# Optimization experiments

Measured on AMD Instinct MI355X. Metric: run time of the kernel, lower is better.

Reference implementation:

```python
import jax, jax.numpy as jnp
import numpy as np

E = 64          # num_experts
DIM = 1024      # model dim
HID = 512       # per-expert FFN hidden dim
N = 65536       # total routed tokens (1024 per expert)


def setup_inputs() -> dict:
    key = jax.random.key(0)
    k_x, k1, k2, k3 = jax.random.split(key, 4)
    x = jax.random.normal(k_x, (N, DIM), dtype=jnp.float32)
    # learned params: w1/w3 [E, HID, DIM], w2 [E, DIM, HID] (trunc_normal std 0.02 ~ normal*0.02)
    w1 = jax.random.normal(k1, (E, HID, DIM), dtype=jnp.float32) * 0.02
    w2 = jax.random.normal(k2, (E, DIM, HID), dtype=jnp.float32) * 0.02
    w3 = jax.random.normal(k3, (E, HID, DIM), dtype=jnp.float32) * 0.02
    num_tokens_per_expert = jnp.full((E,), N // E, dtype=jnp.int32)
    return {"x": x, "w1": w1, "w2": w2, "w3": w3,
            "num_tokens_per_expert": num_tokens_per_expert}


def reference(x, w1, w2, w3, num_tokens_per_expert):
    # Grouped-GEMM SwiGLU expert FFN (torch._grouped_mm path, bf16 compute).
    bf16 = jnp.bfloat16
    xb = x.astype(bf16)                                   # [N, DIM]
    g = num_tokens_per_expert                             # [E] int32 group sizes
    w1t = jnp.swapaxes(w1.astype(bf16), 1, 2)             # [E, DIM, HID]
    w3t = jnp.swapaxes(w3.astype(bf16), 1, 2)             # [E, DIM, HID]
    w2t = jnp.swapaxes(w2.astype(bf16), 1, 2)             # [E, HID, DIM]
    h = jax.nn.silu(jax.lax.ragged_dot(xb, w1t, g))       # [N, HID]
    h = h * jax.lax.ragged_dot(xb, w3t, g)                # fused gate
    out = jax.lax.ragged_dot(h, w2t, g)                   # [N, DIM]
    return out.astype(x.dtype)
```

## Files before the change

kernel.cpp:

```cpp
#include <hip/hip_runtime.h>
#include <hip/hip_bf16.h>
#include <stdint.h>

#define NE   64
#define DIM  1024
#define HID  512
#define TPE  1024

typedef __attribute__((ext_vector_type(8)))  __bf16          bf16x8;
typedef __attribute__((ext_vector_type(16))) float           f32x16;
typedef __attribute__((ext_vector_type(8)))  unsigned short  ushort8_t;
typedef __attribute__((ext_vector_type(4)))  float           float4_t;

__device__ __forceinline__ unsigned short f2bf(float f) {
  return __builtin_bit_cast(unsigned short, static_cast<__bf16>(f));
}
__device__ __forceinline__ float bf2f(unsigned short u) {
  unsigned int x = ((unsigned int)u) << 16;
  return __builtin_bit_cast(float, x);
}
__device__ __forceinline__ ushort8_t pack8(float4_t a, float4_t b) {
  ushort8_t r;
  r[0] = f2bf(a[0]); r[1] = f2bf(a[1]); r[2] = f2bf(a[2]); r[3] = f2bf(a[3]);
  r[4] = f2bf(b[0]); r[5] = f2bf(b[1]); r[6] = f2bf(b[2]); r[7] = f2bf(b[3]);
  return r;
}

#define LDK 40

__device__ __forceinline__ int xcd_swizzle(int bid, int nwg) {
  return (bid & 7) * (nwg >> 3) + (bid >> 3);
}

#define P1_NKT (DIM / 32)

__global__ __launch_bounds__(256, 4) void p1_kernel(
    const float* __restrict__ X, const float* __restrict__ W1,
    const float* __restrict__ W3, unsigned short* __restrict__ H) {
  __shared__ __align__(16) unsigned short lA [2][128 * LDK];
  __shared__ __align__(16) unsigned short lB1[2][ 64 * LDK];
  __shared__ __align__(16) unsigned short lB3[2][ 64 * LDK];

  const int tile = xcd_swizzle(blockIdx.x, NE * 8 * 8);
  const int e  = tile >> 6;
  const int tm = (tile >> 3) & 7;
  const int tn = tile & 7;
  const int t  = threadIdx.x;

  const float* gA  = X  + (size_t)(e * TPE + tm * 128) * DIM;
  const float* gB1 = W1 + ((size_t)e * HID + tn * 64) * DIM;
  const float* gB3 = W3 + ((size_t)e * HID + tn * 64) * DIM;

  float4_t ra[2][2], rb1[2], rb3[2];

  const int arow0 = t >> 2, acol = (t & 3) * 8;
  const int brow  = t >> 2, bcol = (t & 3) * 8;

  auto load_tile = [&](int kt) {
#pragma unroll
    for (int i = 0; i < 2; ++i) {
      const size_t off = (size_t)(arow0 + 64 * i) * DIM + kt * 32 + acol;
      ra[i][0] = *reinterpret_cast<const float4_t*>(gA + off);
      ra[i][1] = *reinterpret_cast<const float4_t*>(gA + off + 4);
    }
    const size_t boff = (size_t)brow * DIM + kt * 32 + bcol;
    rb1[0] = *reinterpret_cast<const float4_t*>(gB1 + boff);
    rb1[1] = *reinterpret_cast<const float4_t*>(gB1 + boff + 4);
    rb3[0] = *reinterpret_cast<const float4_t*>(gB3 + boff);
    rb3[1] = *reinterpret_cast<const float4_t*>(gB3 + boff + 4);
  };
  auto store_tile = [&](int buf) {
#pragma unroll
    for (int i = 0; i < 2; ++i)
      *reinterpret_cast<ushort8_t*>(&lA[buf][(arow0 + 64 * i) * LDK + acol]) =
          pack8(ra[i][0], ra[i][1]);
    *reinterpret_cast<ushort8_t*>(&lB1[buf][brow * LDK + bcol]) = pack8(rb1[0], rb1[1]);
    *reinterpret_cast<ushort8_t*>(&lB3[buf][brow * LDK + bcol]) = pack8(rb3[0], rb3[1]);
  };

  const int lane = t & 63;
  const int wv   = t >> 6;
  const int wr   = wv >> 1, wc = wv & 1;
  const int lr   = lane & 31;
  const int ks   = lane >> 5;

  const int aoff0 = (wr * 64 + lr) * LDK + ks * 8;
  const int boff0 = (wc * 32 + lr) * LDK + ks * 8;

  f32x16 acc1[2], acc3[2];
#pragma unroll
  for (int m = 0; m < 2; ++m)
#pragma unroll
    for (int i = 0; i < 16; ++i) { acc1[m][i] = 0.f; acc3[m][i] = 0.f; }

  load_tile(0);
  for (int kt = 0; kt < P1_NKT; ++kt) {
    const int buf = kt & 1;
    store_tile(buf);
    __syncthreads();
    if (kt + 1 < P1_NKT) load_tile(kt + 1);
#pragma unroll
    for (int kk = 0; kk < 2; ++kk) {
      bf16x8 a[2], b1, b3;
#pragma unroll
      for (int m = 0; m < 2; ++m)
        a[m] = __builtin_bit_cast(bf16x8, *reinterpret_cast<const ushort8_t*>(
                   &lA[buf][aoff0 + m * (32 * LDK) + kk * 16]));
      b1 = __builtin_bit_cast(bf16x8, *reinterpret_cast<const ushort8_t*>(
               &lB1[buf][boff0 + kk * 16]));
      b3 = __builtin_bit_cast(bf16x8, *reinterpret_cast<const ushort8_t*>(
               &lB3[buf][boff0 + kk * 16]));
#pragma unroll
      for (int m = 0; m < 2; ++m) {
        acc1[m] = __builtin_amdgcn_mfma_f32_32x32x16_bf16(a[m], b1, acc1[m], 0, 0, 0);
        acc3[m] = __builtin_amdgcn_mfma_f32_32x32x16_bf16(a[m], b3, acc3[m], 0, 0, 0);
      }
    }
  }

  const int tokBase = e * TPE + tm * 128 + wr * 64;
  const int hid     = tn * 64 + wc * 32 + lr;
#pragma unroll
  for (int m = 0; m < 2; ++m)
#pragma unroll
    for (int r = 0; r < 16; ++r) {
      const int rr  = (r & 3) + 8 * (r >> 2) + 4 * ks;
      const int tok = tokBase + m * 32 + rr;
      const float av = bf2f(f2bf(acc1[m][r]));
      const float bv = bf2f(f2bf(acc3[m][r]));
      const float s  = av / (1.0f + __expf(-av));
      H[(size_t)tok * HID + hid] = f2bf(s * bv);
    }
}

#define P2_NKT (HID / 32)

__global__ __launch_bounds__(256, 4) void p2_kernel(
    const unsigned short* __restrict__ Hin, const float* __restrict__ W2,
    float* __restrict__ OUT) {
  __shared__ __align__(16) unsigned short lA[2][128 * LDK];
  __shared__ __align__(16) unsigned short lB[2][128 * LDK];

  const int tile = xcd_swizzle(blockIdx.x, NE * 8 * 8);
  const int e  = tile >> 6;
  const int tm = (tile >> 3) & 7;
  const int tn = tile & 7;
  const int t  = threadIdx.x;

  const unsigned short* gA = Hin + (size_t)(e * TPE + tm * 128) * HID;
  const float*          gB = W2  + ((size_t)e * DIM + tn * 128) * HID;

  ushort8_t ra[2];
  float4_t  rb[2][2];

  const int row0 = t >> 2, col = (t & 3) * 8;

  auto load_tile = [&](int kt) {
#pragma unroll
    for (int i = 0; i < 2; ++i) {
      ra[i] = *reinterpret_cast<const ushort8_t*>(
          gA + (size_t)(row0 + 64 * i) * HID + kt * 32 + col);
      const size_t off = (size_t)(row0 + 64 * i) * HID + kt * 32 + col;
      rb[i][0] = *reinterpret_cast<const float4_t*>(gB + off);
      rb[i][1] = *reinterpret_cast<const float4_t*>(gB + off + 4);
    }
  };
  auto store_tile = [&](int buf) {
#pragma unroll
    for (int i = 0; i < 2; ++i) {
      const int idx = (row0 + 64 * i) * LDK + col;
      *reinterpret_cast<ushort8_t*>(&lA[buf][idx]) = ra[i];
      *reinterpret_cast<ushort8_t*>(&lB[buf][idx]) = pack8(rb[i][0], rb[i][1]);
    }
  };

  const int lane = t & 63;
  const int wv   = t >> 6;
  const int wr   = wv >> 1, wc = wv & 1;
  const int lr   = lane & 31;
  const int ks   = lane >> 5;

  const int aoff0 = (wr * 64 + lr) * LDK + ks * 8;
  const int boff0 = (wc * 64 + lr) * LDK + ks * 8;

  f32x16 acc[2][2];
#pragma unroll
  for (int m = 0; m < 2; ++m)
#pragma unroll
    for (int n = 0; n < 2; ++n)
#pragma unroll
      for (int i = 0; i < 16; ++i) acc[m][n][i] = 0.f;

  load_tile(0);
  for (int kt = 0; kt < P2_NKT; ++kt) {
    const int buf = kt & 1;
    store_tile(buf);
    __syncthreads();
    if (kt + 1 < P2_NKT) load_tile(kt + 1);
#pragma unroll
    for (int kk = 0; kk < 2; ++kk) {
      bf16x8 a[2], b[2];
#pragma unroll
      for (int m = 0; m < 2; ++m)
        a[m] = __builtin_bit_cast(bf16x8, *reinterpret_cast<const ushort8_t*>(
                   &lA[buf][aoff0 + m * (32 * LDK) + kk * 16]));
#pragma unroll
      for (int n = 0; n < 2; ++n)
        b[n] = __builtin_bit_cast(bf16x8, *reinterpret_cast<const ushort8_t*>(
                   &lB[buf][boff0 + n * (32 * LDK) + kk * 16]));
#pragma unroll
      for (int m = 0; m < 2; ++m)
#pragma unroll
        for (int n = 0; n < 2; ++n)
          acc[m][n] = __builtin_amdgcn_mfma_f32_32x32x16_bf16(a[m], b[n], acc[m][n], 0, 0, 0);
    }
  }

  const int tokBase = e * TPE + tm * 128 + wr * 64;
  const int dBase   = tn * 128 + wc * 64;
#pragma unroll
  for (int m = 0; m < 2; ++m)
#pragma unroll
    for (int n = 0; n < 2; ++n)
#pragma unroll
      for (int r = 0; r < 16; ++r) {
        const int rr  = (r & 3) + 8 * (r >> 2) + 4 * ks;
        const int tok = tokBase + m * 32 + rr;
        const int d   = dBase + n * 32 + lr;
        OUT[(size_t)tok * DIM + d] = bf2f(f2bf(acc[m][n][r]));
      }
}

extern "C" void kernel_launch(void* const* d_in, const int* in_sizes, int n_in,
                              void* d_out, int out_size, void* d_ws, size_t ws_size,
                              hipStream_t stream) {
  (void)in_sizes; (void)n_in; (void)out_size; (void)ws_size;
  const float* X  = (const float*)d_in[0];
  const float* W1 = (const float*)d_in[1];
  const float* W2 = (const float*)d_in[2];
  const float* W3 = (const float*)d_in[3];

  unsigned short* H = (unsigned short*)d_ws;
  float* OUT = (float*)d_out;

  p1_kernel<<<dim3(NE * 8 * 8), dim3(256), 0, stream>>>(X, W1, W3, H);
  p2_kernel<<<dim3(NE * 8 * 8), dim3(256), 0, stream>>>(H, W2, OUT);
}
```

Baseline: 424.7 us.

## Enlarge GEMM tiles to 256-row blocks with 16x16x32 MFMA and 512-thread workgroups

Both GEMM kernels move to 512-thread workgroups with bigger output tiles: 256x128 (gate and up) in the first kernel and 256x128 in the second. Each wave now computes a 64x64 sub-tile with 16x16x32 bf16 MFMAs in place of 32x32x16. The K loop is unrolled by two with two register staging sets. The goal is more operand reuse per global and LDS load, which cuts redundant fp32 reads of X and the weights. The cost is many more accumulator registers, especially in the first kernel (128 floats), which may lower occupancy or cause spills.

```diff
diff --git a/kernel.cpp b/kernel.cpp
--- a/kernel.cpp
+++ b/kernel.cpp
@@ -8,7 +8,7 @@
 #define TPE  1024
 
 typedef __attribute__((ext_vector_type(8)))  __bf16          bf16x8;
-typedef __attribute__((ext_vector_type(16))) float           f32x16;
+typedef __attribute__((ext_vector_type(4)))  float           f32x4;
 typedef __attribute__((ext_vector_type(8)))  unsigned short  ushort8_t;
 typedef __attribute__((ext_vector_type(4)))  float           float4_t;
 
@@ -25,6 +25,9 @@
   r[4] = f2bf(b[0]); r[5] = f2bf(b[1]); r[6] = f2bf(b[2]); r[7] = f2bf(b[3]);
   return r;
 }
+__device__ __forceinline__ bf16x8 ldsfrag(const unsigned short* p) {
+  return __builtin_bit_cast(bf16x8, *reinterpret_cast<const ushort8_t*>(p));
+}
 
 #define LDK 40
 
@@ -34,200 +37,206 @@
 
 #define P1_NKT (DIM / 32)
 
-__global__ __launch_bounds__(256, 4) void p1_kernel(
+__global__ __launch_bounds__(512, 2) void p1_kernel(
     const float* __restrict__ X, const float* __restrict__ W1,
     const float* __restrict__ W3, unsigned short* __restrict__ H) {
-  __shared__ __align__(16) unsigned short lA [2][128 * LDK];
-  __shared__ __align__(16) unsigned short lB1[2][ 64 * LDK];
-  __shared__ __align__(16) unsigned short lB3[2][ 64 * LDK];
-
-  const int tile = xcd_swizzle(blockIdx.x, NE * 8 * 8);
-  const int e  = tile >> 6;
-  const int tm = (tile >> 3) & 7;
-  const int tn = tile & 7;
+  __shared__ __align__(16) unsigned short lA [2][256 * LDK];
+  __shared__ __align__(16) unsigned short lB1[2][128 * LDK];
+  __shared__ __align__(16) unsigned short lB3[2][128 * LDK];
+
+  const int tile = xcd_swizzle(blockIdx.x, NE * 4 * 4);
+  const int e  = tile >> 4;
+  const int tm = (tile >> 2) & 3;
+  const int tn = tile & 3;
   const int t  = threadIdx.x;
 
-  const float* gA  = X  + (size_t)(e * TPE + tm * 128) * DIM;
-  const float* gB1 = W1 + ((size_t)e * HID + tn * 64) * DIM;
-  const float* gB3 = W3 + ((size_t)e * HID + tn * 64) * DIM;
-
-  float4_t ra[2][2], rb1[2], rb3[2];
-
-  const int arow0 = t >> 2, acol = (t & 3) * 8;
-  const int brow  = t >> 2, bcol = (t & 3) * 8;
-
-  auto load_tile = [&](int kt) {
-#pragma unroll
-    for (int i = 0; i < 2; ++i) {
-      const size_t off = (size_t)(arow0 + 64 * i) * DIM + kt * 32 + acol;
-      ra[i][0] = *reinterpret_cast<const float4_t*>(gA + off);
-      ra[i][1] = *reinterpret_cast<const float4_t*>(gA + off + 4);
-    }
-    const size_t boff = (size_t)brow * DIM + kt * 32 + bcol;
-    rb1[0] = *reinterpret_cast<const float4_t*>(gB1 + boff);
-    rb1[1] = *reinterpret_cast<const float4_t*>(gB1 + boff + 4);
-    rb3[0] = *reinterpret_cast<const float4_t*>(gB3 + boff);
-    rb3[1] = *reinterpret_cast<const float4_t*>(gB3 + boff + 4);
-  };
-  auto store_tile = [&](int buf) {
-#pragma unroll
-    for (int i = 0; i < 2; ++i)
-      *reinterpret_cast<ushort8_t*>(&lA[buf][(arow0 + 64 * i) * LDK + acol]) =
-          pack8(ra[i][0], ra[i][1]);
-    *reinterpret_cast<ushort8_t*>(&lB1[buf][brow * LDK + bcol]) = pack8(rb1[0], rb1[1]);
-    *reinterpret_cast<ushort8_t*>(&lB3[buf][brow * LDK + bcol]) = pack8(rb3[0], rb3[1]);
+  const float* gA  = X  + (size_t)(e * TPE + tm * 256) * DIM;
+  const float* gB1 = W1 + ((size_t)e * HID + tn * 128) * DIM;
+  const float* gB3 = W3 + ((size_t)e * HID + tn * 128) * DIM;
+
+  const int arow = t >> 1, acol = (t & 1) * 16;
+  const int brow = t >> 2, bcol = (t & 3) * 8;
+
+  auto load_g = [&](float4_t (&ra)[4], float4_t (&rb1)[2], float4_t (&rb3)[2],
+                    int kt) {
+    const size_t ao = (size_t)arow * DIM + kt * 32 + acol;
+#pragma unroll
+    for (int i = 0; i < 4; ++i)
+      ra[i] = *reinterpret_cast<const float4_t*>(gA + ao + 4 * i);
+    const size_t bo = (size_t)brow * DIM + kt * 32 + bcol;
+    rb1[0] = *reinterpret_cast<const float4_t*>(gB1 + bo);
+    rb1[1] = *reinterpret_cast<const float4_t*>(gB1 + bo + 4);
+    rb3[0] = *reinterpret_cast<const float4_t*>(gB3 + bo);
+    rb3[1] = *reinterpret_cast<const float4_t*>(gB3 + bo + 4);
+  };
+  auto store_l = [&](int buf, float4_t (&ra)[4], float4_t (&rb1)[2],
+                     float4_t (&rb3)[2]) {
+    const int ai = arow * LDK + acol;
+    *reinterpret_cast<ushort8_t*>(&lA[buf][ai])     = pack8(ra[0], ra[1]);
+    *reinterpret_cast<ushort8_t*>(&lA[buf][ai + 8]) = pack8(ra[2], ra[3]);
+    const int bi = brow * LDK + bcol;
+    *reinterpret_cast<ushort8_t*>(&lB1[buf][bi]) = pack8(rb1[0], rb1[1]);
+    *reinterpret_cast<ushort8_t*>(&lB3[buf][bi]) = pack8(rb3[0], rb3[1]);
   };
 
   const int lane = t & 63;
   const int wv   = t >> 6;
   const int wr   = wv >> 1, wc = wv & 1;
-  const int lr   = lane & 31;
-  const int ks   = lane >> 5;
-
-  const int aoff0 = (wr * 64 + lr) * LDK + ks * 8;
-  const int boff0 = (wc * 32 + lr) * LDK + ks * 8;
-
-  f32x16 acc1[2], acc3[2];
-#pragma unroll
-  for (int m = 0; m < 2; ++m)
-#pragma unroll
-    for (int i = 0; i < 16; ++i) { acc1[m][i] = 0.f; acc3[m][i] = 0.f; }
-
-  load_tile(0);
-  for (int kt = 0; kt < P1_NKT; ++kt) {
-    const int buf = kt & 1;
-    store_tile(buf);
-    __syncthreads();
-    if (kt + 1 < P1_NKT) load_tile(kt + 1);
-#pragma unroll
-    for (int kk = 0; kk < 2; ++kk) {
-      bf16x8 a[2], b1, b3;
-#pragma unroll
-      for (int m = 0; m < 2; ++m)
-        a[m] = __builtin_bit_cast(bf16x8, *reinterpret_cast<const ushort8_t*>(
-                   &lA[buf][aoff0 + m * (32 * LDK) + kk * 16]));
-      b1 = __builtin_bit_cast(bf16x8, *reinterpret_cast<const ushort8_t*>(
-               &lB1[buf][boff0 + kk * 16]));
-      b3 = __builtin_bit_cast(bf16x8, *reinterpret_cast<const ushort8_t*>(
-               &lB3[buf][boff0 + kk * 16]));
-#pragma unroll
-      for (int m = 0; m < 2; ++m) {
-        acc1[m] = __builtin_amdgcn_mfma_f32_32x32x16_bf16(a[m], b1, acc1[m], 0, 0, 0);
-        acc3[m] = __builtin_amdgcn_mfma_f32_32x32x16_bf16(a[m], b3, acc3[m], 0, 0, 0);
+  const int fr   = lane & 15;
+  const int ks   = (lane >> 4) * 8;
+
+  f32x4 acc1[4][4], acc3[4][4];
+#pragma unroll
+  for (int mi = 0; mi < 4; ++mi)
+#pragma unroll
+    for (int ni = 0; ni < 4; ++ni)
+#pragma unroll
+      for (int i = 0; i < 4; ++i) { acc1[mi][ni][i] = 0.f; acc3[mi][ni][i] = 0.f; }
+
+  auto mfma_phase = [&](int buf) {
+    bf16x8 b1f[4], b3f[4];
+#pragma unroll
+    for (int ni = 0; ni < 4; ++ni) {
+      const int bi = (wc * 64 + ni * 16 + fr) * LDK + ks;
+      b1f[ni] = ldsfrag(&lB1[buf][bi]);
+      b3f[ni] = ldsfrag(&lB3[buf][bi]);
+    }
+#pragma unroll
+    for (int mi = 0; mi < 4; ++mi) {
+      const bf16x8 af = ldsfrag(&lA[buf][(wr * 64 + mi * 16 + fr) * LDK + ks]);
+#pragma unroll
+      for (int ni = 0; ni < 4; ++ni) {
+        acc1[mi][ni] = __builtin_amdgcn_mfma_f32_16x16x32_bf16(af, b1f[ni], acc1[mi][ni], 0, 0, 0);
+        acc3[mi][ni] = __builtin_amdgcn_mfma_f32_16x16x32_bf16(af, b3f[ni], acc3[mi][ni], 0, 0, 0);
       }
     }
+  };
+
+  float4_t ra0[4], rb10[2], rb30[2];
+  float4_t ra1[4], rb11[2], rb31[2];
+  load_g(ra0, rb10, rb30, 0);
+  load_g(ra1, rb11, rb31, 1);
+
+  for (int kt = 0; kt < P1_NKT; kt += 2) {
+    store_l(0, ra0, rb10, rb30);
+    __syncthreads();
+    if (kt + 2 < P1_NKT) load_g(ra0, rb10, rb30, kt + 2);
+    mfma_phase(0);
+
+    store_l(1, ra1, rb11, rb31);
+    __syncthreads();
+    if (kt + 3 < P1_NKT) load_g(ra1, rb11, rb31, kt + 3);
+    mfma_phase(1);
   }
 
-  const int tokBase = e * TPE + tm * 128 + wr * 64;
-  const int hid     = tn * 64 + wc * 32 + lr;
-#pragma unroll
-  for (int m = 0; m < 2; ++m)
-#pragma unroll
-    for (int r = 0; r < 16; ++r) {
-      const int rr  = (r & 3) + 8 * (r >> 2) + 4 * ks;
-      const int tok = tokBase + m * 32 + rr;
-      const float av = bf2f(f2bf(acc1[m][r]));
-      const float bv = bf2f(f2bf(acc3[m][r]));
-      const float s  = av / (1.0f + __expf(-av));
-      H[(size_t)tok * HID + hid] = f2bf(s * bv);
-    }
+  const int tokBase = e * TPE + tm * 256 + wr * 64;
+  const int hidBase = tn * 128 + wc * 64;
+#pragma unroll
+  for (int mi = 0; mi < 4; ++mi)
+#pragma unroll
+    for (int ni = 0; ni < 4; ++ni)
+#pragma unroll
+      for (int r = 0; r < 4; ++r) {
+        const int tok = tokBase + mi * 16 + (lane >> 4) * 4 + r;
+        const int hid = hidBase + ni * 16 + fr;
+        const float av = bf2f(f2bf(acc1[mi][ni][r]));
+        const float bv = bf2f(f2bf(acc3[mi][ni][r]));
+        const float s  = av / (1.0f + __expf(-av));
+        H[(size_t)tok * HID + hid] = f2bf(s * bv);
+      }
 }
 
 #define P2_NKT (HID / 32)
 
-__global__ __launch_bounds__(256, 4) void p2_kernel(
+__global__ __launch_bounds__(512, 2) void p2_kernel(
     const unsigned short* __restrict__ Hin, const float* __restrict__ W2,
     float* __restrict__ OUT) {
-  __shared__ __align__(16) unsigned short lA[2][128 * LDK];
+  __shared__ __align__(16) unsigned short lA[2][256 * LDK];
   __shared__ __align__(16) unsigned short lB[2][128 * LDK];
 
-  const int tile = xcd_swizzle(blockIdx.x, NE * 8 * 8);
-  const int e  = tile >> 6;
-  const int tm = (tile >> 3) & 7;
+  const int tile = xcd_swizzle(blockIdx.x, NE * 4 * 8);
+  const int e  = tile >> 5;
+  const int tm = (tile >> 3) & 3;
   const int tn = tile & 7;
   const int t  = threadIdx.x;
 
-  const unsigned short* gA = Hin + (size_t)(e * TPE + tm * 128) * HID;
+  const unsigned short* gA = Hin + (size_t)(e * TPE + tm * 256) * HID;
   const float*          gB = W2  + ((size_t)e * DIM + tn * 128) * HID;
 
-  ushort8_t ra[2];
-  float4_t  rb[2][2];
-
-  const int row0 = t >> 2, col = (t & 3) * 8;
-
-  auto load_tile = [&](int kt) {
-#pragma unroll
-    for (int i = 0; i < 2; ++i) {
-      ra[i] = *reinterpret_cast<const ushort8_t*>(
-          gA + (size_t)(row0 + 64 * i) * HID + kt * 32 + col);
-      const size_t off = (size_t)(row0 + 64 * i) * HID + kt * 32 + col;
-      rb[i][0] = *reinterpret_cast<const float4_t*>(gB + off);
-      rb[i][1] = *reinterpret_cast<const float4_t*>(gB + off + 4);
-    }
-  };
-  auto store_tile = [&](int buf) {
-#pragma unroll
-    for (int i = 0; i < 2; ++i) {
-      const int idx = (row0 + 64 * i) * LDK + col;
-      *reinterpret_cast<ushort8_t*>(&lA[buf][idx]) = ra[i];
-      *reinterpret_cast<ushort8_t*>(&lB[buf][idx]) = pack8(rb[i][0], rb[i][1]);
-    }
+  const int arow = t >> 1, acol = (t & 1) * 16;
+  const int brow = t >> 2, bcol = (t & 3) * 8;
+
+  auto load_g = [&](ushort8_t (&ra)[2], float4_t (&rb)[2], int kt) {
+    const size_t ao = (size_t)arow * HID + kt * 32 + acol;
+    ra[0] = *reinterpret_cast<const ushort8_t*>(gA + ao);
+    ra[1] = *reinterpret_cast<const ushort8_t*>(gA + ao + 8);
+    const size_t bo = (size_t)brow * HID + kt * 32 + bcol;
+    rb[0] = *reinterpret_cast<const float4_t*>(gB + bo);
+    rb[1] = *reinterpret_cast<const float4_t*>(gB + bo + 4);
+  };
+  auto store_l = [&](int buf, ushort8_t (&ra)[2], float4_t (&rb)[2]) {
+    const int ai = arow * LDK + acol;
+    *reinterpret_cast<ushort8_t*>(&lA[buf][ai])     = ra[0];
+    *reinterpret_cast<ushort8_t*>(&lA[buf][ai + 8]) = ra[1];
+    *reinterpret_cast<ushort8_t*>(&lB[buf][brow * LDK + bcol]) = pack8(rb[0], rb[1]);
   };
 
   const int lane = t & 63;
   const int wv   = t >> 6;
   const int wr   = wv >> 1, wc = wv & 1;
-  const int lr   = lane & 31;
-  const int ks   = lane >> 5;
-
-  const int aoff0 = (wr * 64 + lr) * LDK + ks * 8;
-  const int boff0 = (wc * 64 + lr) * LDK + ks * 8;
-
-  f32x16 acc[2][2];
-#pragma unroll
-  for (int m = 0; m < 2; ++m)
-#pragma unroll
-    for (int n = 0; n < 2; ++n)
-#pragma unroll
-      for (int i = 0; i < 16; ++i) acc[m][n][i] = 0.f;
-
-  load_tile(0);
-  for (int kt = 0; kt < P2_NKT; ++kt) {
-    const int buf = kt & 1;
-    store_tile(buf);
-    __syncthreads();
-    if (kt + 1 < P2_NKT) load_tile(kt + 1);
-#pragma unroll
-    for (int kk = 0; kk < 2; ++kk) {
-      bf16x8 a[2], b[2];
-#pragma unroll
-      for (int m = 0; m < 2; ++m)
-        a[m] = __builtin_bit_cast(bf16x8, *reinterpret_cast<const ushort8_t*>(
-                   &lA[buf][aoff0 + m * (32 * LDK) + kk * 16]));
-#pragma unroll
-      for (int n = 0; n < 2; ++n)
-        b[n] = __builtin_bit_cast(bf16x8, *reinterpret_cast<const ushort8_t*>(
-                   &lB[buf][boff0 + n * (32 * LDK) + kk * 16]));
-#pragma unroll
-      for (int m = 0; m < 2; ++m)
-#pragma unroll
-        for (int n = 0; n < 2; ++n)
-          acc[m][n] = __builtin_amdgcn_mfma_f32_32x32x16_bf16(a[m], b[n], acc[m][n], 0, 0, 0);
+  const int fr   = lane & 15;
+  const int ks   = (lane >> 4) * 8;
+
+  f32x4 acc[4][4];
+#pragma unroll
+  for (int mi = 0; mi < 4; ++mi)
+#pragma unroll
+    for (int ni = 0; ni < 4; ++ni)
+#pragma unroll
+      for (int i = 0; i < 4; ++i) acc[mi][ni][i] = 0.f;
+
+  auto mfma_phase = [&](int buf) {
+    bf16x8 bfr[4];
+#pragma unroll
+    for (int ni = 0; ni < 4; ++ni)
+      bfr[ni] = ldsfrag(&lB[buf][(wc * 64 + ni * 16 + fr) * LDK + ks]);
+#pragma unroll
+    for (int mi = 0; mi < 4; ++mi) {
+      const bf16x8 af = ldsfrag(&lA[buf][(wr * 64 + mi * 16 + fr) * LDK + ks]);
+#pragma unroll
+      for (int ni = 0; ni < 4; ++ni)
+        acc[mi][ni] = __builtin_amdgcn_mfma_f32_16x16x32_bf16(af, bfr[ni], acc[mi][ni], 0, 0, 0);
     }
+  };
+
+  ushort8_t ra0[2], ra1[2];
+  float4_t  rb0[2], rb1[2];
+  load_g(ra0, rb0, 0);
+  load_g(ra1, rb1, 1);
+
+  for (int kt = 0; kt < P2_NKT; kt += 2) {
+    store_l(0, ra0, rb0);
+    __syncthreads();
+    if (kt + 2 < P2_NKT) load_g(ra0, rb0, kt + 2);
+    mfma_phase(0);
+
+    store_l(1, ra1, rb1);
+    __syncthreads();
+    if (kt + 3 < P2_NKT) load_g(ra1, rb1, kt + 3);
+    mfma_phase(1);
   }
 
-  const int tokBase = e * TPE + tm * 128 + wr * 64;
+  const int tokBase = e * TPE + tm * 256 + wr * 64;
   const int dBase   = tn * 128 + wc * 64;
 #pragma unroll
-  for (int m = 0; m < 2; ++m)
-#pragma unroll
-    for (int n = 0; n < 2; ++n)
-#pragma unroll
-      for (int r = 0; r < 16; ++r) {
-        const int rr  = (r & 3) + 8 * (r >> 2) + 4 * ks;
-        const int tok = tokBase + m * 32 + rr;
-        const int d   = dBase + n * 32 + lr;
-        OUT[(size_t)tok * DIM + d] = bf2f(f2bf(acc[m][n][r]));
+  for (int mi = 0; mi < 4; ++mi)
+#pragma unroll
+    for (int ni = 0; ni < 4; ++ni)
+#pragma unroll
+      for (int r = 0; r < 4; ++r) {
+        const int tok = tokBase + mi * 16 + (lane >> 4) * 4 + r;
+        const int d   = dBase + ni * 16 + fr;
+        OUT[(size_t)tok * DIM + d] = bf2f(f2bf(acc[mi][ni][r]));
       }
 }
 
@@ -243,6 +252,6 @@
   unsigned short* H = (unsigned short*)d_ws;
   float* OUT = (float*)d_out;
 
-  p1_kernel<<<dim3(NE * 8 * 8), dim3(256), 0, stream>>>(X, W1, W3, H);
-  p2_kernel<<<dim3(NE * 8 * 8), dim3(256), 0, stream>>>(H, W2, OUT);
-}
+  p1_kernel<<<dim3(NE * 4 * 4), dim3(512), 0, stream>>>(X, W1, W3, H);
+  p2_kernel<<<dim3(NE * 4 * 8), dim3(512), 0, stream>>>(H, W2, OUT);
+}
```

New measurement: 449.7 us. 1.06x slower.

## Deepen register prefetch to two tiles and use LDS-only barriers in both GEMMs

Applied to the files above, without the earlier changes.

Both kernels now keep two sets of staging registers so global loads run two k-tiles ahead. They replace __syncthreads with a barrier that waits only on LDS counters, so in-flight global loads can overlap the MFMA phase instead of being drained at each barrier. The tile index mapping is changed so consecutive blocks share a weight slice rather than an activation slice. The P2 activation load now uses two 16-byte loads per thread over 128 rows. The extra staging registers raise register pressure, and launch bounds drop from 4 to 3 blocks per CU to make room, which risks lower occupancy.

```diff
diff --git a/kernel.cpp b/kernel.cpp
--- a/kernel.cpp
+++ b/kernel.cpp
@@ -25,6 +25,14 @@
   r[4] = f2bf(b[0]); r[5] = f2bf(b[1]); r[6] = f2bf(b[2]); r[7] = f2bf(b[3]);
   return r;
 }
+__device__ __forceinline__ bf16x8 ldsfrag(const unsigned short* p) {
+  return __builtin_bit_cast(bf16x8, *reinterpret_cast<const ushort8_t*>(p));
+}
+
+__device__ __forceinline__ void barrier_lgkm() {
+  asm volatile("s_waitcnt lgkmcnt(0)" ::: "memory");
+  __builtin_amdgcn_s_barrier();
+}
 
 #define LDK 40
 
@@ -34,7 +42,7 @@
 
 #define P1_NKT (DIM / 32)
 
-__global__ __launch_bounds__(256, 4) void p1_kernel(
+__global__ __launch_bounds__(256, 3) void p1_kernel(
     const float* __restrict__ X, const float* __restrict__ W1,
     const float* __restrict__ W3, unsigned short* __restrict__ H) {
   __shared__ __align__(16) unsigned short lA [2][128 * LDK];
@@ -43,49 +51,48 @@
 
   const int tile = xcd_swizzle(blockIdx.x, NE * 8 * 8);
   const int e  = tile >> 6;
-  const int tm = (tile >> 3) & 7;
-  const int tn = tile & 7;
+  const int tn = (tile >> 3) & 7;
+  const int tm = tile & 7;
   const int t  = threadIdx.x;
 
   const float* gA  = X  + (size_t)(e * TPE + tm * 128) * DIM;
   const float* gB1 = W1 + ((size_t)e * HID + tn * 64) * DIM;
   const float* gB3 = W3 + ((size_t)e * HID + tn * 64) * DIM;
 
-  float4_t ra[2][2], rb1[2], rb3[2];
-
-  const int arow0 = t >> 2, acol = (t & 3) * 8;
-  const int brow  = t >> 2, bcol = (t & 3) * 8;
-
-  auto load_tile = [&](int kt) {
+  const int ar = t >> 2, ac = (t & 3) * 8;
+
+  float4_t a0[2][2], b10[2], b30[2];
+  float4_t a1[2][2], b11[2], b31[2];
+
+  auto load_g = [&](float4_t (&a)[2][2], float4_t (&b1)[2], float4_t (&b3)[2],
+                    int kt) {
 #pragma unroll
     for (int i = 0; i < 2; ++i) {
-      const size_t off = (size_t)(arow0 + 64 * i) * DIM + kt * 32 + acol;
-      ra[i][0] = *reinterpret_cast<const float4_t*>(gA + off);
-      ra[i][1] = *reinterpret_cast<const float4_t*>(gA + off + 4);
-    }
-    const size_t boff = (size_t)brow * DIM + kt * 32 + bcol;
-    rb1[0] = *reinterpret_cast<const float4_t*>(gB1 + boff);
-    rb1[1] = *reinterpret_cast<const float4_t*>(gB1 + boff + 4);
-    rb3[0] = *reinterpret_cast<const float4_t*>(gB3 + boff);
-    rb3[1] = *reinterpret_cast<const float4_t*>(gB3 + boff + 4);
-  };
-  auto store_tile = [&](int buf) {
+      const size_t o = (size_t)(ar + 64 * i) * DIM + kt * 32 + ac;
+      a[i][0] = *reinterpret_cast<const float4_t*>(gA + o);
+      a[i][1] = *reinterpret_cast<const float4_t*>(gA + o + 4);
+    }
+    const size_t ob = (size_t)ar * DIM + kt * 32 + ac;
+    b1[0] = *reinterpret_cast<const float4_t*>(gB1 + ob);
+    b1[1] = *reinterpret_cast<const float4_t*>(gB1 + ob + 4);
+    b3[0] = *reinterpret_cast<const float4_t*>(gB3 + ob);
+    b3[1] = *reinterpret_cast<const float4_t*>(gB3 + ob + 4);
+  };
+  auto store_l = [&](int buf, float4_t (&a)[2][2], float4_t (&b1)[2],
+                     float4_t (&b3)[2]) {
 #pragma unroll
     for (int i = 0; i < 2; ++i)
-      *reinterpret_cast<ushort8_t*>(&lA[buf][(arow0 + 64 * i) * LDK + acol]) =
-          pack8(ra[i][0], ra[i][1]);
-    *reinterpret_cast<ushort8_t*>(&lB1[buf][brow * LDK + bcol]) = pack8(rb1[0], rb1[1]);
-    *reinterpret_cast<ushort8_t*>(&lB3[buf][brow * LDK + bcol]) = pack8(rb3[0], rb3[1]);
+      *reinterpret_cast<ushort8_t*>(&lA[buf][(ar + 64 * i) * LDK + ac]) =
+          pack8(a[i][0], a[i][1]);
+    *reinterpret_cast<ushort8_t*>(&lB1[buf][ar * LDK + ac]) = pack8(b1[0], b1[1]);
+    *reinterpret_cast<ushort8_t*>(&lB3[buf][ar * LDK + ac]) = pack8(b3[0], b3[1]);
   };
 
   const int lane = t & 63;
   const int wv   = t >> 6;
   const int wr   = wv >> 1, wc = wv & 1;
   const int lr   = lane & 31;
-  const int ks   = lane >> 5;
-
-  const int aoff0 = (wr * 64 + lr) * LDK + ks * 8;
-  const int boff0 = (wc * 32 + lr) * LDK + ks * 8;
+  const int ks   = (lane >> 5) * 8;
 
   f32x16 acc1[2], acc3[2];
 #pragma unroll
@@ -93,38 +100,44 @@
 #pragma unroll
     for (int i = 0; i < 16; ++i) { acc1[m][i] = 0.f; acc3[m][i] = 0.f; }
 
-  load_tile(0);
-  for (int kt = 0; kt < P1_NKT; ++kt) {
-    const int buf = kt & 1;
-    store_tile(buf);
-    __syncthreads();
-    if (kt + 1 < P1_NKT) load_tile(kt + 1);
+  auto mfma_phase = [&](int buf) {
 #pragma unroll
     for (int kk = 0; kk < 2; ++kk) {
-      bf16x8 a[2], b1, b3;
+      bf16x8 am[2];
 #pragma unroll
       for (int m = 0; m < 2; ++m)
-        a[m] = __builtin_bit_cast(bf16x8, *reinterpret_cast<const ushort8_t*>(
-                   &lA[buf][aoff0 + m * (32 * LDK) + kk * 16]));
-      b1 = __builtin_bit_cast(bf16x8, *reinterpret_cast<const ushort8_t*>(
-               &lB1[buf][boff0 + kk * 16]));
-      b3 = __builtin_bit_cast(bf16x8, *reinterpret_cast<const ushort8_t*>(
-               &lB3[buf][boff0 + kk * 16]));
+        am[m] = ldsfrag(&lA[buf][(wr * 64 + m * 32 + lr) * LDK + kk * 16 + ks]);
+      const bf16x8 b1 = ldsfrag(&lB1[buf][(wc * 32 + lr) * LDK + kk * 16 + ks]);
+      const bf16x8 b3 = ldsfrag(&lB3[buf][(wc * 32 + lr) * LDK + kk * 16 + ks]);
 #pragma unroll
       for (int m = 0; m < 2; ++m) {
-        acc1[m] = __builtin_amdgcn_mfma_f32_32x32x16_bf16(a[m], b1, acc1[m], 0, 0, 0);
-        acc3[m] = __builtin_amdgcn_mfma_f32_32x32x16_bf16(a[m], b3, acc3[m], 0, 0, 0);
+        acc1[m] = __builtin_amdgcn_mfma_f32_32x32x16_bf16(am[m], b1, acc1[m], 0, 0, 0);
+        acc3[m] = __builtin_amdgcn_mfma_f32_32x32x16_bf16(am[m], b3, acc3[m], 0, 0, 0);
       }
     }
+  };
+
+  load_g(a0, b10, b30, 0);
+  load_g(a1, b11, b31, 1);
+  for (int kt = 0; kt < P1_NKT; kt += 2) {
+    store_l(0, a0, b10, b30);
+    if (kt + 2 < P1_NKT) load_g(a0, b10, b30, kt + 2);
+    barrier_lgkm();
+    mfma_phase(0);
+    store_l(1, a1, b11, b31);
+    if (kt + 3 < P1_NKT) load_g(a1, b11, b31, kt + 3);
+    barrier_lgkm();
+    mfma_phase(1);
   }
 
   const int tokBase = e * TPE + tm * 128 + wr * 64;
   const int hid     = tn * 64 + wc * 32 + lr;
+  const int ks4     = (lane >> 5) * 4;
 #pragma unroll
   for (int m = 0; m < 2; ++m)
 #pragma unroll
     for (int r = 0; r < 16; ++r) {
-      const int rr  = (r & 3) + 8 * (r >> 2) + 4 * ks;
+      const int rr  = (r & 3) + 8 * (r >> 2) + ks4;
       const int tok = tokBase + m * 32 + rr;
       const float av = bf2f(f2bf(acc1[m][r]));
       const float bv = bf2f(f2bf(acc3[m][r]));
@@ -135,7 +148,7 @@
 
 #define P2_NKT (HID / 32)
 
-__global__ __launch_bounds__(256, 4) void p2_kernel(
+__global__ __launch_bounds__(256, 3) void p2_kernel(
     const unsigned short* __restrict__ Hin, const float* __restrict__ W2,
     float* __restrict__ OUT) {
   __shared__ __align__(16) unsigned short lA[2][128 * LDK];
@@ -143,45 +156,45 @@
 
   const int tile = xcd_swizzle(blockIdx.x, NE * 8 * 8);
   const int e  = tile >> 6;
-  const int tm = (tile >> 3) & 7;
-  const int tn = tile & 7;
+  const int tn = (tile >> 3) & 7;
+  const int tm = tile & 7;
   const int t  = threadIdx.x;
 
   const unsigned short* gA = Hin + (size_t)(e * TPE + tm * 128) * HID;
   const float*          gB = W2  + ((size_t)e * DIM + tn * 128) * HID;
 
-  ushort8_t ra[2];
-  float4_t  rb[2][2];
-
-  const int row0 = t >> 2, col = (t & 3) * 8;
-
-  auto load_tile = [&](int kt) {
+  const int arow = t >> 1, acol = (t & 1) * 16;
+  const int br = t >> 2, bc = (t & 3) * 8;
+
+  ushort8_t ha0[2], ha1[2];
+  float4_t  wb0[2][2], wb1[2][2];
+
+  auto load_g = [&](ushort8_t (&ha)[2], float4_t (&wb)[2][2], int kt) {
+    const size_t ao = (size_t)arow * HID + kt * 32 + acol;
+    ha[0] = *reinterpret_cast<const ushort8_t*>(gA + ao);
+    ha[1] = *reinterpret_cast<const ushort8_t*>(gA + ao + 8);
 #pragma unroll
     for (int i = 0; i < 2; ++i) {
-      ra[i] = *reinterpret_cast<const ushort8_t*>(
-          gA + (size_t)(row0 + 64 * i) * HID + kt * 32 + col);
-      const size_t off = (size_t)(row0 + 64 * i) * HID + kt * 32 + col;
-      rb[i][0] = *reinterpret_cast<const float4_t*>(gB + off);
-      rb[i][1] = *reinterpret_cast<const float4_t*>(gB + off + 4);
-    }
-  };
-  auto store_tile = [&](int buf) {
-#pragma unroll
-    for (int i = 0; i < 2; ++i) {
-      const int idx = (row0 + 64 * i) * LDK + col;
-      *reinterpret_cast<ushort8_t*>(&lA[buf][idx]) = ra[i];
-      *reinterpret_cast<ushort8_t*>(&lB[buf][idx]) = pack8(rb[i][0], rb[i][1]);
-    }
+      const size_t bo = (size_t)(br + 64 * i) * HID + kt * 32 + bc;
+      wb[i][0] = *reinterpret_cast<const float4_t*>(gB + bo);
+      wb[i][1] = *reinterpret_cast<const float4_t*>(gB + bo + 4);
+    }
+  };
+  auto store_l = [&](int buf, ushort8_t (&ha)[2], float4_t (&wb)[2][2]) {
+    const int ai = arow * LDK + acol;
+    *reinterpret_cast<ushort8_t*>(&lA[buf][ai])     = ha[0];
+    *reinterpret_cast<ushort8_t*>(&lA[buf][ai + 8]) = ha[1];
+#pragma unroll
+    for (int i = 0; i < 2; ++i)
+      *reinterpret_cast<ushort8_t*>(&lB[buf][(br + 64 * i) * LDK + bc]) =
+          pack8(wb[i][0], wb[i][1]);
   };
 
   const int lane = t & 63;
   const int wv   = t >> 6;
   const int wr   = wv >> 1, wc = wv & 1;
   const int lr   = lane & 31;
-  const int ks   = lane >> 5;
-
-  const int aoff0 = (wr * 64 + lr) * LDK + ks * 8;
-  const int boff0 = (wc * 64 + lr) * LDK + ks * 8;
+  const int ks   = (lane >> 5) * 8;
 
   f32x16 acc[2][2];
 #pragma unroll
@@ -191,40 +204,48 @@
 #pragma unroll
       for (int i = 0; i < 16; ++i) acc[m][n][i] = 0.f;
 
-  load_tile(0);
-  for (int kt = 0; kt < P2_NKT; ++kt) {
-    const int buf = kt & 1;
-    store_tile(buf);
-    __syncthreads();
-    if (kt + 1 < P2_NKT) load_tile(kt + 1);
+  auto mfma_phase = [&](int buf) {
 #pragma unroll
     for (int kk = 0; kk < 2; ++kk) {
-      bf16x8 a[2], b[2];
+      bf16x8 am[2], bn[2];
 #pragma unroll
       for (int m = 0; m < 2; ++m)
-        a[m] = __builtin_bit_cast(bf16x8, *reinterpret_cast<const ushort8_t*>(
-                   &lA[buf][aoff0 + m * (32 * LDK) + kk * 16]));
+        am[m] = ldsfrag(&lA[buf][(wr * 64 + m * 32 + lr) * LDK + kk * 16 + ks]);
 #pragma unroll
       for (int n = 0; n < 2; ++n)
-        b[n] = __builtin_bit_cast(bf16x8, *reinterpret_cast<const ushort8_t*>(
-                   &lB[buf][boff0 + n * (32 * LDK) + kk * 16]));
+        bn[n] = ldsfrag(&lB[buf][(wc * 64 + n * 32 + lr) * LDK + kk * 16 + ks]);
 #pragma unroll
       for (int m = 0; m < 2; ++m)
 #pragma unroll
         for (int n = 0; n < 2; ++n)
-          acc[m][n] = __builtin_amdgcn_mfma_f32_32x32x16_bf16(a[m], b[n], acc[m][n], 0, 0, 0);
-    }
+          acc[m][n] = __builtin_amdgcn_mfma_f32_32x32x16_bf16(am[m], bn[n], acc[m][n], 0, 0, 0);
+    }
+  };
+
+  load_g(ha0, wb0, 0);
+  load_g(ha1, wb1, 1);
+  for (int kt = 0; kt < P2_NKT; kt += 2) {
+    store_l(0, ha0, wb0);
+    if (kt + 2 < P2_NKT) load_g(ha0, wb0, kt + 2);
+    barrier_lgkm();
+    mfma_phase(0);
+
+    store_l(1, ha1, wb1);
+    if (kt + 3 < P2_NKT) load_g(ha1, wb1, kt + 3);
+    barrier_lgkm();
+    mfma_phase(1);
   }
 
   const int tokBase = e * TPE + tm * 128 + wr * 64;
   const int dBase   = tn * 128 + wc * 64;
+  const int ks4     = (lane >> 5) * 4;
 #pragma unroll
   for (int m = 0; m < 2; ++m)
 #pragma unroll
     for (int n = 0; n < 2; ++n)
 #pragma unroll
       for (int r = 0; r < 16; ++r) {
-        const int rr  = (r & 3) + 8 * (r >> 2) + 4 * ks;
+        const int rr  = (r & 3) + 8 * (r >> 2) + ks4;
         const int tok = tokBase + m * 32 + rr;
         const int d   = dBase + n * 32 + lr;
         OUT[(size_t)tok * DIM + d] = bf2f(f2bf(acc[m][n][r]));
```

Result: slower. 520.3 us (+22.5%).
